# Kernel tuning notes

Measured on AMD Instinct MI355X. Metric: run time of the kernel, lower is better.

Reference implementation:

```python
import jax, jax.numpy as jnp
import numpy as np

EMBED_DIM = 1024
HEAD_SIZE = 64
N_HEAD = 16
N_QUERY_GROUPS = 4
SEQ_LEN = 2048
BATCH = 8


def setup_inputs() -> dict:
    key = jax.random.key(0)
    ks = jax.random.split(key, 7)
    s = 1.0 / np.sqrt(EMBED_DIM)
    x = jax.random.normal(ks[0], (BATCH, SEQ_LEN, EMBED_DIM), dtype=jnp.float32)
    Wq = jax.random.uniform(ks[1], (EMBED_DIM, N_HEAD * HEAD_SIZE), jnp.float32, -s, s)
    bq = jax.random.uniform(ks[2], (N_HEAD * HEAD_SIZE,), jnp.float32, -s, s)
    Wk = jax.random.uniform(ks[3], (EMBED_DIM, N_QUERY_GROUPS * HEAD_SIZE), jnp.float32, -s, s)
    bk = jax.random.uniform(ks[4], (N_QUERY_GROUPS * HEAD_SIZE,), jnp.float32, -s, s)
    Wv = jax.random.uniform(ks[5], (EMBED_DIM, N_QUERY_GROUPS * HEAD_SIZE), jnp.float32, -s, s)
    bv = jax.random.uniform(ks[6], (N_QUERY_GROUPS * HEAD_SIZE,), jnp.float32, -s, s)
    return {"x": x, "Wq": Wq, "bq": bq, "Wk": Wk, "bk": bk, "Wv": Wv, "bv": bv}


def reference(x, Wq, bq, Wk, bk, Wv, bv):
    B, T, _ = x.shape
    rep = N_HEAD // N_QUERY_GROUPS  # queries per group
    Q = x @ Wq + bq  # (B, T, H*hs)
    # GQA: torch .repeat tiles the group-block [g0..g3, g0..g3, ...]
    K = (x @ Wk + bk).reshape(B, T, N_QUERY_GROUPS, HEAD_SIZE)
    K = jnp.tile(K, (1, 1, rep, 1)).reshape(B, T, N_HEAD * HEAD_SIZE)
    V = (x @ Wv + bv).reshape(B, T, N_QUERY_GROUPS, HEAD_SIZE)
    V = jnp.tile(V, (1, 1, rep, 1)).reshape(B, T, N_HEAD * HEAD_SIZE)
    # flattened-head scores: contract over full H*hs dim (as in source)
    att = jnp.einsum('btd,bsd->bts', Q, K)  # (B, T, T)
    causal = jnp.triu(jnp.ones((T, T), dtype=bool), k=1)
    mask = jnp.where(causal, jnp.float32(-jnp.inf), jnp.float32(0.0))[None, None]  # (1,1,T,T)
    att = att + mask  # broadcasts to (1, B, T, T), matching torch semantics
    att = jax.nn.softmax(att, axis=-1) / jnp.sqrt(jnp.float32(HEAD_SIZE))  # post-hoc scale, as in source
    out = jnp.einsum('xbts,bsd->xbtd', att, V)  # (1, B, T, H*hs)
    return out
```

## Files before the change

kernel.cpp:

```cpp
#include <hip/hip_runtime.h>
#include <float.h>
#include <stdint.h>

#define T_ 2048
#define DG 256

typedef _Float16 half8 __attribute__((ext_vector_type(8)));
typedef _Float16 half4v __attribute__((ext_vector_type(4)));
typedef __fp16 fp16x2 __attribute__((ext_vector_type(2)));
typedef float f32x4 __attribute__((ext_vector_type(4)));
typedef float f32x16 __attribute__((ext_vector_type(16)));
typedef unsigned uint2v __attribute__((ext_vector_type(2)));

__device__ __forceinline__ void gload16(const void* g, void* l) {
  __builtin_amdgcn_global_load_lds(
      (const __attribute__((address_space(1))) unsigned int*)g,
      (__attribute__((address_space(3))) unsigned int*)l, 16, 0, 0);
}
#define WAIT_LGKM0() do { asm volatile("s_waitcnt lgkmcnt(0)" ::: "memory"); __builtin_amdgcn_sched_barrier(0); } while (0)

__device__ __forceinline__ float cross32(float x, int g) {
  unsigned u = __builtin_bit_cast(unsigned, x);
  uint2v r = __builtin_amdgcn_permlane32_swap(u, u, false, false);
  return __builtin_bit_cast(float, g ? r[0] : r[1]);
}

__global__ __launch_bounds__(256) void prep_w(
    const float* __restrict__ Wq, const float* __restrict__ bq,
    const float* __restrict__ Wk, const float* __restrict__ bk,
    const float* __restrict__ Wv, const float* __restrict__ bv,
    _Float16* __restrict__ Wt, float* __restrict__ bcat) {
  for (int idx = blockIdx.x * 256 + threadIdx.x; idx < 786432; idx += 768 * 256) {
    int n = idx >> 10, k = idx & 1023;
    float v;
    if (n < 256)      v = Wq[k * 1024 + n] + Wq[k * 1024 + n + 256]
                        + Wq[k * 1024 + n + 512] + Wq[k * 1024 + n + 768];
    else if (n < 512) v = Wk[k * 256 + n - 256];
    else              v = Wv[k * 256 + n - 512];
    Wt[idx] = (_Float16)v;
    if (k == 0) {
      float bb;
      if (n < 256)      bb = bq[n] + bq[n + 256] + bq[n + 512] + bq[n + 768];
      else if (n < 512) bb = bk[n - 256];
      else              bb = bv[n - 512];
      bcat[n] = bb;
    }
  }
}

__global__ __launch_bounds__(256) void xcvt(const float* __restrict__ x,
                                            _Float16* __restrict__ xh) {
  size_t i = (size_t)blockIdx.x * 256 + threadIdx.x;
  const float4* s = (const float4*)x + i * 2;
  float4 a = s[0], b = s[1];
  half8 h;
  h[0] = (_Float16)a.x; h[1] = (_Float16)a.y; h[2] = (_Float16)a.z; h[3] = (_Float16)a.w;
  h[4] = (_Float16)b.x; h[5] = (_Float16)b.y; h[6] = (_Float16)b.z; h[7] = (_Float16)b.w;
  *(half8*)(xh + i * 8) = h;
}

__global__ __launch_bounds__(256) void qkv_gemm(
    const _Float16* __restrict__ xh, const _Float16* __restrict__ Wt,
    const float* __restrict__ bcat,
    _Float16* __restrict__ Qh, _Float16* __restrict__ Kf, _Float16* __restrict__ Vf) {
  __shared__ __align__(16) uint8_t smem[32768];
  const int tid = threadIdx.x;
  const int w = tid >> 6, l = tid & 63;
  const int wr = w >> 1, wc = w & 1;
  const int lr = l & 15, lk = l >> 4;
  const int m0 = blockIdx.x * 128;
  const int by = blockIdx.y >> 1;
  const int nh = blockIdx.y & 1;

  f32x4 acc[4][4] = {};

  auto stage = [&](int k0, int buf) {
    uint8_t* Ab = smem + buf * 16384;
    uint8_t* Bb = Ab + 8192;
#pragma unroll
    for (int i = 0; i < 2; ++i) {
      int si = i * 256 + tid;
      int row = si >> 2, p = si & 3;
      gload16(xh + (size_t)(m0 + row) * 1024 + k0 + ((p ^ (row & 3)) << 3), Ab + si * 16);
    }
#pragma unroll
    for (int i = 0; i < 2; ++i) {
      int si = i * 256 + tid;
      int row = si >> 2, p = si & 3;
      gload16(Wt + (size_t)(by * 256 + nh * 128 + row) * 1024 + k0 + ((p ^ (row & 3)) << 3),
              Bb + si * 16);
    }
  };

  stage(0, 0);
  __syncthreads();

  for (int kt = 0; kt < 32; ++kt) {
    int cur = kt & 1;
    if (kt < 31) stage((kt + 1) * 32, cur ^ 1);
    const uint8_t* Ab = smem + cur * 16384;
    const uint8_t* Bb = Ab + 8192;
    half8 af[4], bf[4];
#pragma unroll
    for (int mi = 0; mi < 4; ++mi) {
      int row = wr * 64 + mi * 16 + lr;
      af[mi] = *(const half8*)(Ab + row * 64 + ((lk ^ (row & 3)) << 4));
    }
#pragma unroll
    for (int ni = 0; ni < 4; ++ni) {
      int row = wc * 64 + ni * 16 + lr;
      bf[ni] = *(const half8*)(Bb + row * 64 + ((lk ^ (row & 3)) << 4));
    }
#pragma unroll
    for (int mi = 0; mi < 4; ++mi)
#pragma unroll
      for (int ni = 0; ni < 4; ++ni)
        acc[mi][ni] = __builtin_amdgcn_mfma_f32_16x16x32_f16(af[mi], bf[ni], acc[mi][ni], 0, 0, 0);
    __syncthreads();
  }

  if (by == 0) {
#pragma unroll
    for (int mi = 0; mi < 4; ++mi)
#pragma unroll
      for (int ni = 0; ni < 4; ++ni) {
        int nl = nh * 128 + wc * 64 + ni * 16 + lr;
        int mg = m0 + wr * 64 + mi * 16 + lk * 4;
        float bias = bcat[nl];
#pragma unroll
        for (int r = 0; r < 4; ++r)
          Qh[(size_t)(mg + r) * DG + nl] = (_Float16)((acc[mi][ni][r] + bias) * 1.44269504f);
      }
  } else if (by == 2) {
#pragma unroll
    for (int mi = 0; mi < 4; ++mi)
#pragma unroll
      for (int ni = 0; ni < 4; ++ni) {
        int nl = nh * 128 + wc * 64 + ni * 16 + lr;
        int mg = m0 + wr * 64 + mi * 16 + lk * 4;
        float bias = bcat[512 + nl];
        int dt = nl >> 5, lnv = nl & 31;
        int bb = mg >> 11, t0 = mg & 2047;
        int st = t0 >> 5, sp = t0 & 31;
        int hs = sp >> 4, gg = (sp >> 3) & 1, j0 = sp & 7;
        size_t idx = (size_t)(((bb * 64 + st) * 8 + dt) * 2 + hs) * 512
                   + (gg * 32 + lnv) * 8 + j0;
        half4v h;
#pragma unroll
        for (int r = 0; r < 4; ++r) h[r] = (_Float16)(acc[mi][ni][r] + bias);
        *(half4v*)(Vf + idx) = h;
      }
  } else {
#pragma unroll
    for (int mi = 0; mi < 4; ++mi)
#pragma unroll
      for (int ni = 0; ni < 4; ++ni) {
        int dl = wc * 64 + ni * 16 + lr;
        float bias = bcat[256 + nh * 128 + dl];
#pragma unroll
        for (int r = 0; r < 4; ++r) {
          int t = wr * 64 + mi * 16 + lk * 4 + r;
          *(_Float16*)(smem + t * 256 + ((dl * 2) ^ ((t & 7) << 4))) =
              (_Float16)(acc[mi][ni][r] + bias);
        }
      }
    __syncthreads();
#pragma unroll
    for (int i = 0; i < 8; ++i) {
      int p = i * 256 + tid;
      int ln = p & 31, g = (p >> 5) & 1, cl = (p >> 6) & 7, st = p >> 9;
      int t = st * 32 + ln;
      int d0 = cl * 16 + g * 8;
      half8 v = *(const half8*)(smem + t * 256 + ((d0 * 2) ^ ((t & 7) << 4)));
      int tg = m0 + t;
      int bb = tg >> 11, stg = (tg & 2047) >> 5;
      int cc = nh * 8 + cl;
      *(half8*)(Kf + ((size_t)(((bb * 64 + stg) * 16 + cc) * 2 + g) * 32 + ln) * 8) = v;
    }
  }
}

__global__ __launch_bounds__(256, 4) void attn_main(
    const _Float16* __restrict__ Qg, const _Float16* __restrict__ Kf,
    const _Float16* __restrict__ Vf, float* __restrict__ out,
    _Float16* __restrict__ PO, float* __restrict__ ML) {
  __shared__ float Sx[5120];
  const int tid = threadIdx.x;
  const int wv = tid >> 6;
  const int l  = tid & 63;
  const int g  = l >> 5;
  const int ln = l & 31;
  const int id = blockIdx.x;
  const int b  = id & 7;
  const int u  = id >> 3;
  int tt, nc, c;
  if (u < 16)      { tt = u;                  nc = 1; c = 0; }
  else if (u < 48) { tt = 16 + ((u - 16) >> 1); nc = 2; c = (u - 16) & 1; }
  else if (u < 96) { tt = 32 + (u - 48) / 3;  nc = 3; c = (u - 48) % 3; }
  else             { tt = 48 + ((u - 96) >> 2); nc = 4; c = (u - 96) & 3; }
  const int len = (tt + nc) / nc;
  const int lo  = c * len;
  const int hi  = min(lo + len, tt + 1);
  const int q0  = tt * 32;

  const _Float16* Kfb = Kf + (size_t)b * 524288;
  const _Float16* Vfb = Vf + (size_t)b * 524288;

  const _Float16* Qrow = Qg + ((size_t)(b * T_ + q0 + ln)) * DG + wv * 64 + 8 * g;
  half8 qf[4];
#pragma unroll
  for (int j = 0; j < 4; ++j) qf[j] = *(const half8*)(Qrow + j * 16);

  f32x16 o0 = {}, o1 = {};
  float m_r = -1e30f, l_r = 0.0f;

  for (int kt = lo; kt < hi; ++kt) {
    const _Float16* kbase = Kfb + (size_t)(kt * 16 + 4 * wv) * 512 + l * 8;
    half8 kf0 = *(const half8*)(kbase);
    half8 kf1 = *(const half8*)(kbase + 512);
    half8 kf2 = *(const half8*)(kbase + 1024);
    half8 kf3 = *(const half8*)(kbase + 1536);
    const _Float16* vbase = Vfb + (size_t)(kt * 8 + 2 * wv) * 1024 + l * 8;
    half8 va0 = *(const half8*)(vbase);
    half8 va1 = *(const half8*)(vbase + 512);
    half8 vb0 = *(const half8*)(vbase + 1024);
    half8 vb1 = *(const half8*)(vbase + 1536);

    f32x16 s_acc = {};
    __builtin_amdgcn_s_setprio(1);
    s_acc = __builtin_amdgcn_mfma_f32_32x32x16_f16(kf0, qf[0], s_acc, 0, 0, 0);
    s_acc = __builtin_amdgcn_mfma_f32_32x32x16_f16(kf1, qf[1], s_acc, 0, 0, 0);
    s_acc = __builtin_amdgcn_mfma_f32_32x32x16_f16(kf2, qf[2], s_acc, 0, 0, 0);
    s_acc = __builtin_amdgcn_mfma_f32_32x32x16_f16(kf3, qf[3], s_acc, 0, 0, 0);
    __builtin_amdgcn_s_setprio(0);

    {
      float* myrow = Sx + (wv * 64 + l) * 20;
#pragma unroll
      for (int i = 0; i < 4; ++i)
        *(f32x4*)(myrow + 4 * i) = *(((const f32x4*)&s_acc) + i);
    }
    WAIT_LGKM0();
    __builtin_amdgcn_s_barrier();

    f32x4 sv[4];
#pragma unroll
    for (int i = 0; i < 4; ++i) sv[i] = *(((const f32x4*)&s_acc) + i);
#pragma unroll
    for (int wo = 0; wo < 4; ++wo) {
      if (wo == wv) continue;
      const float* prow = Sx + (wo * 64 + l) * 20;
#pragma unroll
      for (int i = 0; i < 4; ++i) sv[i] += *(const f32x4*)(prow + 4 * i);
    }
    float s[16];
#pragma unroll
    for (int r = 0; r < 16; ++r) s[r] = sv[r >> 2][r & 3];

    if (kt == tt) {
#pragma unroll
      for (int r = 0; r < 16; ++r) {
        int srow = (r & 3) + 8 * (r >> 2) + 4 * g;
        if (srow > ln) s[r] = -1e30f;
      }
    }
    float pmax = s[0];
#pragma unroll
    for (int r = 1; r < 16; ++r) pmax = fmaxf(pmax, s[r]);
    pmax = fmaxf(pmax, cross32(pmax, g));
    if (!__all(pmax <= m_r + 8.0f)) {
      float mnew = fmaxf(m_r, pmax);
      float sc = __builtin_amdgcn_exp2f(m_r - mnew);
      l_r *= sc;
#pragma unroll
      for (int r = 0; r < 16; ++r) { o0[r] *= sc; o1[r] *= sc; }
      m_r = mnew;
    }
    float p[16]; float psum = 0.0f;
#pragma unroll
    for (int r = 0; r < 16; ++r) { p[r] = __builtin_amdgcn_exp2f(s[r] - m_r); psum += p[r]; }
    l_r += psum + cross32(psum, g);

    unsigned ph[8];
#pragma unroll
    for (int i = 0; i < 8; ++i) {
      fp16x2 t2 = __builtin_amdgcn_cvt_pkrtz(p[2 * i], p[2 * i + 1]);
      ph[i] = __builtin_bit_cast(unsigned, t2);
    }
    union U { unsigned u[4]; half8 h; };
    U f0, f1;
    {
      uint2v r02 = __builtin_amdgcn_permlane32_swap(ph[0], ph[2], false, false);
      uint2v r13 = __builtin_amdgcn_permlane32_swap(ph[1], ph[3], false, false);
      uint2v r46 = __builtin_amdgcn_permlane32_swap(ph[4], ph[6], false, false);
      uint2v r57 = __builtin_amdgcn_permlane32_swap(ph[5], ph[7], false, false);
      f0.u[0] = r02[0]; f0.u[2] = r02[1];
      f0.u[1] = r13[0]; f0.u[3] = r13[1];
      f1.u[0] = r46[0]; f1.u[2] = r46[1];
      f1.u[1] = r57[0]; f1.u[3] = r57[1];
    }

    __builtin_amdgcn_s_setprio(1);
    o0 = __builtin_amdgcn_mfma_f32_32x32x16_f16(va0, f0.h, o0, 0, 0, 0);
    o0 = __builtin_amdgcn_mfma_f32_32x32x16_f16(va1, f1.h, o0, 0, 0, 0);
    o1 = __builtin_amdgcn_mfma_f32_32x32x16_f16(vb0, f0.h, o1, 0, 0, 0);
    o1 = __builtin_amdgcn_mfma_f32_32x32x16_f16(vb1, f1.h, o1, 0, 0, 0);
    __builtin_amdgcn_s_setprio(0);

    __builtin_amdgcn_s_barrier();
  }

  float* chunk = Sx + wv * 1280;
  if (nc == 1) {
    float inv = 1.0f / (l_r * 8.0f);
    float* ob = out + ((size_t)(b * T_ + q0)) * 1024;
#pragma unroll
    for (int dtl = 0; dtl < 2; ++dtl) {
      const f32x16& oo = dtl ? o1 : o0;
      WAIT_LGKM0();
#pragma unroll
      for (int r = 0; r < 16; ++r) {
        int dl = (r & 3) + 8 * (r >> 2) + 4 * g;
        chunk[ln * 33 + dl] = oo[r] * inv;
      }
      WAIT_LGKM0();
#pragma unroll
      for (int rr = 0; rr < 2; ++rr) {
        int qq = (l >> 2) + 16 * rr;
        int cp = (l & 3) * 8;
        float vv[8];
#pragma unroll
        for (int jj = 0; jj < 8; ++jj) vv[jj] = chunk[qq * 33 + cp + jj];
        float4 w0 = make_float4(vv[0], vv[1], vv[2], vv[3]);
        float4 w1 = make_float4(vv[4], vv[5], vv[6], vv[7]);
        float* orow = ob + (size_t)qq * 1024 + (2 * wv + dtl) * 32 + cp;
#pragma unroll
        for (int rep = 0; rep < 4; ++rep) {
          *(float4*)(orow + rep * 256)     = w0;
          *(float4*)(orow + rep * 256 + 4) = w1;
        }
      }
    }
  } else {
    int ti = tt - 16;
    int off = (ti < 16) ? ti * 2 : (ti < 32) ? 32 + (ti - 16) * 3 : 80 + (ti - 32) * 4;
    int slot = b * 144 + off + c;
    _Float16* P = PO + (size_t)slot * 8192;
#pragma unroll
    for (int dtl = 0; dtl < 2; ++dtl) {
      const f32x16& oo = dtl ? o1 : o0;
      WAIT_LGKM0();
#pragma unroll
      for (int r = 0; r < 16; ++r) {
        int dl = (r & 3) + 8 * (r >> 2) + 4 * g;
        chunk[ln * 33 + dl] = oo[r];
      }
      WAIT_LGKM0();
#pragma unroll
      for (int rr = 0; rr < 2; ++rr) {
        int qq = (l >> 2) + 16 * rr;
        int cp = (l & 3) * 8;
        half8 hv;
#pragma unroll
        for (int jj = 0; jj < 8; ++jj) hv[jj] = (_Float16)chunk[qq * 33 + cp + jj];
        *(half8*)(P + qq * 256 + (2 * wv + dtl) * 32 + cp) = hv;
      }
    }
    if (wv == 0 && l < 32) {
      ML[(size_t)slot * 64 + l]      = m_r;
      ML[(size_t)slot * 64 + 32 + l] = l_r;
    }
  }
}

__global__ __launch_bounds__(256) void attn_merge(
    const _Float16* __restrict__ PO, const float* __restrict__ ML,
    float* __restrict__ out) {
  const int id = blockIdx.x;
  const int b = id & 7, ti = id >> 3;
  const int tt = 16 + ti;
  const int nc = (ti < 16) ? 2 : (ti < 32) ? 3 : 4;
  const int off = (ti < 16) ? ti * 2 : (ti < 32) ? 32 + (ti - 16) * 3 : 80 + (ti - 32) * 4;
  const int slot0 = b * 144 + off;
  const int tid = threadIdx.x;
  const int row = tid >> 3, cb = tid & 7;

  float mj[4], lj[4];
  float M = -1e30f;
#pragma unroll
  for (int j = 0; j < 4; ++j)
    if (j < nc) {
      mj[j] = ML[(size_t)(slot0 + j) * 64 + row];
      lj[j] = ML[(size_t)(slot0 + j) * 64 + 32 + row];
      M = fmaxf(M, mj[j]);
    }
  float sc[4], lsum = 0.0f;
#pragma unroll
  for (int j = 0; j < 4; ++j)
    if (j < nc) { sc[j] = __builtin_amdgcn_exp2f(mj[j] - M); lsum += lj[j] * sc[j]; }
  float inv = 1.0f / (lsum * 8.0f);

  float acc[32] = {};
#pragma unroll
  for (int j = 0; j < 4; ++j)
    if (j < nc) {
      const _Float16* P = PO + (size_t)(slot0 + j) * 8192 + row * 256 + cb * 32;
      float s = sc[j];
#pragma unroll
      for (int q = 0; q < 4; ++q) {
        half8 h = *(const half8*)(P + q * 8);
#pragma unroll
        for (int e = 0; e < 8; ++e) acc[q * 8 + e] += s * (float)h[e];
      }
    }
  float* orow = out + ((size_t)(b * T_ + tt * 32 + row)) * 1024 + cb * 32;
#pragma unroll
  for (int q = 0; q < 8; ++q) {
    float4 v;
    v.x = acc[q * 4 + 0] * inv; v.y = acc[q * 4 + 1] * inv;
    v.z = acc[q * 4 + 2] * inv; v.w = acc[q * 4 + 3] * inv;
#pragma unroll
    for (int rep = 0; rep < 4; ++rep)
      *(float4*)(orow + rep * 256 + q * 4) = v;
  }
}

extern "C" void kernel_launch(void* const* d_in, const int* in_sizes, int n_in,
                              void* d_out, int out_size, void* d_ws, size_t ws_size,
                              hipStream_t stream) {
  const float* x  = (const float*)d_in[0];
  const float* Wq = (const float*)d_in[1];
  const float* bq = (const float*)d_in[2];
  const float* Wk = (const float*)d_in[3];
  const float* bk = (const float*)d_in[4];
  const float* Wv = (const float*)d_in[5];
  const float* bv = (const float*)d_in[6];
  float* out = (float*)d_out;
  char* ws = (char*)d_ws;
  _Float16* Wt   = (_Float16*)ws;
  float*    bcat = (float*)(ws + 0x180000);
  _Float16* Qh   = (_Float16*)(ws + 0x181000);
  _Float16* Kf   = (_Float16*)(ws + 0x981000);
  _Float16* Vf   = (_Float16*)(ws + 0x1181000);
  _Float16* xh   = (_Float16*)(ws + 0x1981000);
  _Float16* PO   = (_Float16*)(ws + 0x1981000);
  float*    ML   = (float*)(ws + 0x1981000 + 0x1200000);

  prep_w<<<768, 256, 0, stream>>>(Wq, bq, Wk, bk, Wv, bv, Wt, bcat);
  xcvt<<<8192, 256, 0, stream>>>(x, xh);
  qkv_gemm<<<dim3(128, 6), 256, 0, stream>>>(xh, Wt, bcat, Qh, Kf, Vf);
  attn_main<<<1280, 256, 0, stream>>>(Qh, Kf, Vf, out, PO, ML);
  attn_merge<<<384, 256, 0, stream>>>(PO, ML, out);
}
```

Before: 156.8 us.

## Fuse fp32-to-fp16 conversion of x into QKV GEMM and widen N tile

Removes the separate xcvt kernel and its fp16 copy of x: the GEMM now reads fp32 x through registers, converts with packed round-toward-zero conversions, and writes the fp16 tile to LDS one iteration ahead. The N tile doubles to 256 so each block covers a whole Q/K/V section, which halves the grid and means x is read from global memory once per section instead of twice. This trades a full extra pass over x for more accumulator registers, a larger LDS footprint, fewer blocks, and a two-phase K epilogue. The conversion also changes rounding from round-to-nearest to round-toward-zero.

```diff
diff --git a/kernel.cpp b/kernel.cpp
--- a/kernel.cpp
+++ b/kernel.cpp
@@ -23,6 +23,15 @@
   unsigned u = __builtin_bit_cast(unsigned, x);
   uint2v r = __builtin_amdgcn_permlane32_swap(u, u, false, false);
   return __builtin_bit_cast(float, g ? r[0] : r[1]);
+}
+
+__device__ __forceinline__ half8 cvt8(float4 a, float4 b) {
+  union { unsigned u[4]; half8 h; } r;
+  r.u[0] = __builtin_bit_cast(unsigned, __builtin_amdgcn_cvt_pkrtz(a.x, a.y));
+  r.u[1] = __builtin_bit_cast(unsigned, __builtin_amdgcn_cvt_pkrtz(a.z, a.w));
+  r.u[2] = __builtin_bit_cast(unsigned, __builtin_amdgcn_cvt_pkrtz(b.x, b.y));
+  r.u[3] = __builtin_bit_cast(unsigned, __builtin_amdgcn_cvt_pkrtz(b.z, b.w));
+  return r.h;
 }
 
 __global__ __launch_bounds__(256) void prep_w(
@@ -48,74 +57,74 @@
   }
 }
 
-__global__ __launch_bounds__(256) void xcvt(const float* __restrict__ x,
-                                            _Float16* __restrict__ xh) {
-  size_t i = (size_t)blockIdx.x * 256 + threadIdx.x;
-  const float4* s = (const float4*)x + i * 2;
-  float4 a = s[0], b = s[1];
-  half8 h;
-  h[0] = (_Float16)a.x; h[1] = (_Float16)a.y; h[2] = (_Float16)a.z; h[3] = (_Float16)a.w;
-  h[4] = (_Float16)b.x; h[5] = (_Float16)b.y; h[6] = (_Float16)b.z; h[7] = (_Float16)b.w;
-  *(half8*)(xh + i * 8) = h;
-}
-
 __global__ __launch_bounds__(256) void qkv_gemm(
-    const _Float16* __restrict__ xh, const _Float16* __restrict__ Wt,
+    const float* __restrict__ x, const _Float16* __restrict__ Wt,
     const float* __restrict__ bcat,
     _Float16* __restrict__ Qh, _Float16* __restrict__ Kf, _Float16* __restrict__ Vf) {
-  __shared__ __align__(16) uint8_t smem[32768];
+  __shared__ __align__(16) uint8_t smem[49152];
   const int tid = threadIdx.x;
   const int w = tid >> 6, l = tid & 63;
   const int wr = w >> 1, wc = w & 1;
   const int lr = l & 15, lk = l >> 4;
   const int m0 = blockIdx.x * 128;
-  const int by = blockIdx.y >> 1;
-  const int nh = blockIdx.y & 1;
-
-  f32x4 acc[4][4] = {};
-
-  auto stage = [&](int k0, int buf) {
-    uint8_t* Ab = smem + buf * 16384;
-    uint8_t* Bb = Ab + 8192;
-#pragma unroll
-    for (int i = 0; i < 2; ++i) {
+  const int by = blockIdx.y;
+  const int n0 = by * 256;
+
+  f32x4 acc[4][8] = {};
+
+  const int arow = tid >> 1;
+  const int ag   = (tid & 1) * 2;
+
+  auto loadA = [&](int k0, float4* fr) {
+    const float4* src = (const float4*)(x + (size_t)(m0 + arow) * 1024 + k0 + ag * 8);
+    fr[0] = src[0]; fr[1] = src[1]; fr[2] = src[2]; fr[3] = src[3];
+  };
+  auto writeA = [&](int buf, const float4* fr) {
+    uint8_t* Ab = smem + buf * 24576;
+    *(half8*)(Ab + arow * 64 + (((ag + 0) ^ (arow & 3)) << 4)) = cvt8(fr[0], fr[1]);
+    *(half8*)(Ab + arow * 64 + (((ag + 1) ^ (arow & 3)) << 4)) = cvt8(fr[2], fr[3]);
+  };
+  auto stageB = [&](int k0, int buf) {
+    uint8_t* Bb = smem + buf * 24576 + 8192;
+#pragma unroll
+    for (int i = 0; i < 4; ++i) {
       int si = i * 256 + tid;
       int row = si >> 2, p = si & 3;
-      gload16(xh + (size_t)(m0 + row) * 1024 + k0 + ((p ^ (row & 3)) << 3), Ab + si * 16);
-    }
-#pragma unroll
-    for (int i = 0; i < 2; ++i) {
-      int si = i * 256 + tid;
-      int row = si >> 2, p = si & 3;
-      gload16(Wt + (size_t)(by * 256 + nh * 128 + row) * 1024 + k0 + ((p ^ (row & 3)) << 3),
-              Bb + si * 16);
+      gload16(Wt + (size_t)(n0 + row) * 1024 + k0 + ((p ^ (row & 3)) << 3), Bb + si * 16);
     }
   };
 
-  stage(0, 0);
+  {
+    float4 fr[4];
+    loadA(0, fr);
+    stageB(0, 0);
+    writeA(0, fr);
+  }
   __syncthreads();
 
   for (int kt = 0; kt < 32; ++kt) {
     int cur = kt & 1;
-    if (kt < 31) stage((kt + 1) * 32, cur ^ 1);
-    const uint8_t* Ab = smem + cur * 16384;
+    float4 nf[4];
+    if (kt < 31) { loadA((kt + 1) * 32, nf); stageB((kt + 1) * 32, cur ^ 1); }
+    const uint8_t* Ab = smem + cur * 24576;
     const uint8_t* Bb = Ab + 8192;
-    half8 af[4], bf[4];
+    half8 af[4], bf[8];
 #pragma unroll
     for (int mi = 0; mi < 4; ++mi) {
       int row = wr * 64 + mi * 16 + lr;
       af[mi] = *(const half8*)(Ab + row * 64 + ((lk ^ (row & 3)) << 4));
     }
 #pragma unroll
-    for (int ni = 0; ni < 4; ++ni) {
-      int row = wc * 64 + ni * 16 + lr;
+    for (int ni = 0; ni < 8; ++ni) {
+      int row = wc * 128 + ni * 16 + lr;
       bf[ni] = *(const half8*)(Bb + row * 64 + ((lk ^ (row & 3)) << 4));
     }
 #pragma unroll
     for (int mi = 0; mi < 4; ++mi)
 #pragma unroll
-      for (int ni = 0; ni < 4; ++ni)
+      for (int ni = 0; ni < 8; ++ni)
         acc[mi][ni] = __builtin_amdgcn_mfma_f32_16x16x32_f16(af[mi], bf[ni], acc[mi][ni], 0, 0, 0);
+    if (kt < 31) writeA(cur ^ 1, nf);
     __syncthreads();
   }
 
@@ -123,8 +132,8 @@
 #pragma unroll
     for (int mi = 0; mi < 4; ++mi)
 #pragma unroll
-      for (int ni = 0; ni < 4; ++ni) {
-        int nl = nh * 128 + wc * 64 + ni * 16 + lr;
+      for (int ni = 0; ni < 8; ++ni) {
+        int nl = wc * 128 + ni * 16 + lr;
         int mg = m0 + wr * 64 + mi * 16 + lk * 4;
         float bias = bcat[nl];
 #pragma unroll
@@ -135,8 +144,8 @@
 #pragma unroll
     for (int mi = 0; mi < 4; ++mi)
 #pragma unroll
-      for (int ni = 0; ni < 4; ++ni) {
-        int nl = nh * 128 + wc * 64 + ni * 16 + lr;
+      for (int ni = 0; ni < 8; ++ni) {
+        int nl = wc * 128 + ni * 16 + lr;
         int mg = m0 + wr * 64 + mi * 16 + lk * 4;
         float bias = bcat[512 + nl];
         int dt = nl >> 5, lnv = nl & 31;
@@ -152,30 +161,36 @@
       }
   } else {
 #pragma unroll
-    for (int mi = 0; mi < 4; ++mi)
-#pragma unroll
-      for (int ni = 0; ni < 4; ++ni) {
-        int dl = wc * 64 + ni * 16 + lr;
-        float bias = bcat[256 + nh * 128 + dl];
-#pragma unroll
-        for (int r = 0; r < 4; ++r) {
-          int t = wr * 64 + mi * 16 + lk * 4 + r;
-          *(_Float16*)(smem + t * 256 + ((dl * 2) ^ ((t & 7) << 4))) =
-              (_Float16)(acc[mi][ni][r] + bias);
-        }
-      }
-    __syncthreads();
-#pragma unroll
-    for (int i = 0; i < 8; ++i) {
-      int p = i * 256 + tid;
-      int ln = p & 31, g = (p >> 5) & 1, cl = (p >> 6) & 7, st = p >> 9;
-      int t = st * 32 + ln;
-      int d0 = cl * 16 + g * 8;
-      half8 v = *(const half8*)(smem + t * 256 + ((d0 * 2) ^ ((t & 7) << 4)));
-      int tg = m0 + t;
-      int bb = tg >> 11, stg = (tg & 2047) >> 5;
-      int cc = nh * 8 + cl;
-      *(half8*)(Kf + ((size_t)(((bb * 64 + stg) * 16 + cc) * 2 + g) * 32 + ln) * 8) = v;
+    for (int h = 0; h < 2; ++h) {
+      if (wc == h) {
+#pragma unroll
+        for (int mi = 0; mi < 4; ++mi)
+#pragma unroll
+          for (int ni = 0; ni < 8; ++ni) {
+            int dl = ni * 16 + lr;
+            float bias = bcat[256 + h * 128 + dl];
+#pragma unroll
+            for (int r = 0; r < 4; ++r) {
+              int t = wr * 64 + mi * 16 + lk * 4 + r;
+              *(_Float16*)(smem + t * 256 + ((dl * 2) ^ ((t & 7) << 4))) =
+                  (_Float16)(acc[mi][ni][r] + bias);
+            }
+          }
+      }
+      __syncthreads();
+#pragma unroll
+      for (int i = 0; i < 8; ++i) {
+        int p = i * 256 + tid;
+        int ln = p & 31, g = (p >> 5) & 1, cl = (p >> 6) & 7, st = p >> 9;
+        int t = st * 32 + ln;
+        int d0 = cl * 16 + g * 8;
+        half8 v = *(const half8*)(smem + t * 256 + ((d0 * 2) ^ ((t & 7) << 4)));
+        int tg = m0 + t;
+        int bb = tg >> 11, stg = (tg & 2047) >> 5;
+        int cc = h * 8 + cl;
+        *(half8*)(Kf + ((size_t)(((bb * 64 + stg) * 16 + cc) * 2 + g) * 32 + ln) * 8) = v;
+      }
+      __syncthreads();
     }
   }
 }
@@ -442,13 +457,11 @@
   _Float16* Qh   = (_Float16*)(ws + 0x181000);
   _Float16* Kf   = (_Float16*)(ws + 0x981000);
   _Float16* Vf   = (_Float16*)(ws + 0x1181000);
-  _Float16* xh   = (_Float16*)(ws + 0x1981000);
   _Float16* PO   = (_Float16*)(ws + 0x1981000);
   float*    ML   = (float*)(ws + 0x1981000 + 0x1200000);
 
   prep_w<<<768, 256, 0, stream>>>(Wq, bq, Wk, bk, Wv, bv, Wt, bcat);
-  xcvt<<<8192, 256, 0, stream>>>(x, xh);
-  qkv_gemm<<<dim3(128, 6), 256, 0, stream>>>(xh, Wt, bcat, Qh, Kf, Vf);
+  qkv_gemm<<<dim3(128, 3), 256, 0, stream>>>(x, Wt, bcat, Qh, Kf, Vf);
   attn_main<<<1280, 256, 0, stream>>>(Qh, Kf, Vf, out, PO, ML);
   attn_merge<<<384, 256, 0, stream>>>(PO, ML, out);
 }
```

Result: slower. 185.6 us (+18.3%).

## Fuse weight prep into x conversion; centralize softmax in wave 0 with LDS broadcast

Applied to the files above, without the earlier changes.

Merges the weight-transpose/fold kernel into the x fp16 conversion kernel, removing one launch. In attention, only wave 0 reduces the split-K score partials and computes the softmax. It then publishes the fp16 probabilities, rescale factors and a rescale flag through shared memory, and the other waves read them after an extra barrier. This removes redundant softmax work across four waves, but adds a second block barrier per key tile and serializes the softmax on one wave.

```diff
diff --git a/kernel.cpp b/kernel.cpp
--- a/kernel.cpp
+++ b/kernel.cpp
@@ -25,19 +25,27 @@
   return __builtin_bit_cast(float, g ? r[0] : r[1]);
 }
 
-__global__ __launch_bounds__(256) void prep_w(
+__global__ __launch_bounds__(256) void prepx(
+    const float* __restrict__ x,
     const float* __restrict__ Wq, const float* __restrict__ bq,
     const float* __restrict__ Wk, const float* __restrict__ bk,
     const float* __restrict__ Wv, const float* __restrict__ bv,
-    _Float16* __restrict__ Wt, float* __restrict__ bcat) {
-  for (int idx = blockIdx.x * 256 + threadIdx.x; idx < 786432; idx += 768 * 256) {
-    int n = idx >> 10, k = idx & 1023;
+    _Float16* __restrict__ xh, _Float16* __restrict__ Wt, float* __restrict__ bcat) {
+  size_t t = (size_t)blockIdx.x * 256 + threadIdx.x;
+  const float4* s = (const float4*)x + t * 2;
+  float4 a = s[0], b = s[1];
+  half8 h;
+  h[0] = (_Float16)a.x; h[1] = (_Float16)a.y; h[2] = (_Float16)a.z; h[3] = (_Float16)a.w;
+  h[4] = (_Float16)b.x; h[5] = (_Float16)b.y; h[6] = (_Float16)b.z; h[7] = (_Float16)b.w;
+  *(half8*)(xh + t * 8) = h;
+  if (t < 786432) {
+    int n = (int)(t >> 10), k = (int)(t & 1023);
     float v;
     if (n < 256)      v = Wq[k * 1024 + n] + Wq[k * 1024 + n + 256]
                         + Wq[k * 1024 + n + 512] + Wq[k * 1024 + n + 768];
     else if (n < 512) v = Wk[k * 256 + n - 256];
     else              v = Wv[k * 256 + n - 512];
-    Wt[idx] = (_Float16)v;
+    Wt[t] = (_Float16)v;
     if (k == 0) {
       float bb;
       if (n < 256)      bb = bq[n] + bq[n + 256] + bq[n + 512] + bq[n + 768];
@@ -46,17 +54,6 @@
       bcat[n] = bb;
     }
   }
-}
-
-__global__ __launch_bounds__(256) void xcvt(const float* __restrict__ x,
-                                            _Float16* __restrict__ xh) {
-  size_t i = (size_t)blockIdx.x * 256 + threadIdx.x;
-  const float4* s = (const float4*)x + i * 2;
-  float4 a = s[0], b = s[1];
-  half8 h;
-  h[0] = (_Float16)a.x; h[1] = (_Float16)a.y; h[2] = (_Float16)a.z; h[3] = (_Float16)a.w;
-  h[4] = (_Float16)b.x; h[5] = (_Float16)b.y; h[6] = (_Float16)b.z; h[7] = (_Float16)b.w;
-  *(half8*)(xh + i * 8) = h;
 }
 
 __global__ __launch_bounds__(256) void qkv_gemm(
@@ -185,6 +182,10 @@
     const _Float16* __restrict__ Vf, float* __restrict__ out,
     _Float16* __restrict__ PO, float* __restrict__ ML) {
   __shared__ float Sx[5120];
+  __shared__ __align__(16) _Float16 Pl[1024];
+  __shared__ float SC[64];
+  __shared__ float INV[64];
+  __shared__ int Flg;
   const int tid = threadIdx.x;
   const int wv = tid >> 6;
   const int l  = tid & 63;
@@ -234,7 +235,7 @@
     s_acc = __builtin_amdgcn_mfma_f32_32x32x16_f16(kf3, qf[3], s_acc, 0, 0, 0);
     __builtin_amdgcn_s_setprio(0);
 
-    {
+    if (wv != 0) {
       float* myrow = Sx + (wv * 64 + l) * 20;
 #pragma unroll
       for (int i = 0; i < 4; ++i)
@@ -243,76 +244,109 @@
     WAIT_LGKM0();
     __builtin_amdgcn_s_barrier();
 
-    f32x4 sv[4];
-#pragma unroll
-    for (int i = 0; i < 4; ++i) sv[i] = *(((const f32x4*)&s_acc) + i);
-#pragma unroll
-    for (int wo = 0; wo < 4; ++wo) {
-      if (wo == wv) continue;
-      const float* prow = Sx + (wo * 64 + l) * 20;
-#pragma unroll
-      for (int i = 0; i < 4; ++i) sv[i] += *(const f32x4*)(prow + 4 * i);
-    }
-    float s[16];
-#pragma unroll
-    for (int r = 0; r < 16; ++r) s[r] = sv[r >> 2][r & 3];
-
-    if (kt == tt) {
-#pragma unroll
-      for (int r = 0; r < 16; ++r) {
-        int srow = (r & 3) + 8 * (r >> 2) + 4 * g;
-        if (srow > ln) s[r] = -1e30f;
-      }
-    }
-    float pmax = s[0];
-#pragma unroll
-    for (int r = 1; r < 16; ++r) pmax = fmaxf(pmax, s[r]);
-    pmax = fmaxf(pmax, cross32(pmax, g));
-    if (!__all(pmax <= m_r + 8.0f)) {
-      float mnew = fmaxf(m_r, pmax);
-      float sc = __builtin_amdgcn_exp2f(m_r - mnew);
-      l_r *= sc;
-#pragma unroll
-      for (int r = 0; r < 16; ++r) { o0[r] *= sc; o1[r] *= sc; }
-      m_r = mnew;
-    }
-    float p[16]; float psum = 0.0f;
-#pragma unroll
-    for (int r = 0; r < 16; ++r) { p[r] = __builtin_amdgcn_exp2f(s[r] - m_r); psum += p[r]; }
-    l_r += psum + cross32(psum, g);
-
-    unsigned ph[8];
-#pragma unroll
-    for (int i = 0; i < 8; ++i) {
-      fp16x2 t2 = __builtin_amdgcn_cvt_pkrtz(p[2 * i], p[2 * i + 1]);
-      ph[i] = __builtin_bit_cast(unsigned, t2);
-    }
-    union U { unsigned u[4]; half8 h; };
-    U f0, f1;
-    {
-      uint2v r02 = __builtin_amdgcn_permlane32_swap(ph[0], ph[2], false, false);
-      uint2v r13 = __builtin_amdgcn_permlane32_swap(ph[1], ph[3], false, false);
-      uint2v r46 = __builtin_amdgcn_permlane32_swap(ph[4], ph[6], false, false);
-      uint2v r57 = __builtin_amdgcn_permlane32_swap(ph[5], ph[7], false, false);
-      f0.u[0] = r02[0]; f0.u[2] = r02[1];
-      f0.u[1] = r13[0]; f0.u[3] = r13[1];
-      f1.u[0] = r46[0]; f1.u[2] = r46[1];
-      f1.u[1] = r57[0]; f1.u[3] = r57[1];
+    half8 f0h, f1h;
+    if (wv == 0) {
+      f32x4 sv[4];
+#pragma unroll
+      for (int i = 0; i < 4; ++i) sv[i] = *(((const f32x4*)&s_acc) + i);
+#pragma unroll
+      for (int wo = 1; wo < 4; ++wo) {
+        const float* prow = Sx + (wo * 64 + l) * 20;
+#pragma unroll
+        for (int i = 0; i < 4; ++i) sv[i] += *(const f32x4*)(prow + 4 * i);
+      }
+      float s[16];
+#pragma unroll
+      for (int r = 0; r < 16; ++r) s[r] = sv[r >> 2][r & 3];
+      if (kt == tt) {
+#pragma unroll
+        for (int r = 0; r < 16; ++r) {
+          int srow = (r & 3) + 8 * (r >> 2) + 4 * g;
+          if (srow > ln) s[r] = -1e30f;
+        }
+      }
+      float pmax = s[0];
+#pragma unroll
+      for (int r = 1; r < 16; ++r) pmax = fmaxf(pmax, s[r]);
+      pmax = fmaxf(pmax, cross32(pmax, g));
+      int doresc = !__all(pmax <= m_r + 8.0f);
+      float scl = 1.0f;
+      if (doresc) {
+        float mnew = fmaxf(m_r, pmax);
+        scl = __builtin_amdgcn_exp2f(m_r - mnew);
+        l_r *= scl;
+#pragma unroll
+        for (int r = 0; r < 16; ++r) { o0[r] *= scl; o1[r] *= scl; }
+        m_r = mnew;
+      }
+      if (l == 0) Flg = doresc;
+      SC[l] = scl;
+      float p[16]; float psum = 0.0f;
+#pragma unroll
+      for (int r = 0; r < 16; ++r) { p[r] = __builtin_amdgcn_exp2f(s[r] - m_r); psum += p[r]; }
+      l_r += psum + cross32(psum, g);
+      unsigned ph[8];
+#pragma unroll
+      for (int i = 0; i < 8; ++i) {
+        fp16x2 t2 = __builtin_amdgcn_cvt_pkrtz(p[2 * i], p[2 * i + 1]);
+        ph[i] = __builtin_bit_cast(unsigned, t2);
+      }
+      union U { unsigned u[4]; half8 h; };
+      U w0, w1;
+      w0.u[0] = ph[0]; w0.u[1] = ph[1]; w0.u[2] = ph[2]; w0.u[3] = ph[3];
+      w1.u[0] = ph[4]; w1.u[1] = ph[5]; w1.u[2] = ph[6]; w1.u[3] = ph[7];
+      *(half8*)&Pl[l * 16]     = w0.h;
+      *(half8*)&Pl[l * 16 + 8] = w1.h;
+      U f0, f1;
+      {
+        uint2v r02 = __builtin_amdgcn_permlane32_swap(ph[0], ph[2], false, false);
+        uint2v r13 = __builtin_amdgcn_permlane32_swap(ph[1], ph[3], false, false);
+        uint2v r46 = __builtin_amdgcn_permlane32_swap(ph[4], ph[6], false, false);
+        uint2v r57 = __builtin_amdgcn_permlane32_swap(ph[5], ph[7], false, false);
+        f0.u[0] = r02[0]; f0.u[2] = r02[1];
+        f0.u[1] = r13[0]; f0.u[3] = r13[1];
+        f1.u[0] = r46[0]; f1.u[2] = r46[1];
+        f1.u[1] = r57[0]; f1.u[3] = r57[1];
+      }
+      f0h = f0.h; f1h = f1.h;
+    }
+    WAIT_LGKM0();
+    __builtin_amdgcn_s_barrier();
+
+    if (wv != 0) {
+      int dr = Flg;
+      if (dr) {
+        float scl = SC[l];
+#pragma unroll
+        for (int r = 0; r < 16; ++r) { o0[r] *= scl; o1[r] *= scl; }
+      }
+      union V8 { half4v v[2]; half8 h; } F0, F1;
+      const _Float16* base0 = &Pl[ln * 16];
+      const _Float16* base1 = &Pl[(32 + ln) * 16];
+      F0.v[0] = *(const half4v*)(base0 + 4 * g);
+      F0.v[1] = *(const half4v*)(base1 + 4 * g);
+      F1.v[0] = *(const half4v*)(base0 + 8 + 4 * g);
+      F1.v[1] = *(const half4v*)(base1 + 8 + 4 * g);
+      f0h = F0.h; f1h = F1.h;
     }
 
     __builtin_amdgcn_s_setprio(1);
-    o0 = __builtin_amdgcn_mfma_f32_32x32x16_f16(va0, f0.h, o0, 0, 0, 0);
-    o0 = __builtin_amdgcn_mfma_f32_32x32x16_f16(va1, f1.h, o0, 0, 0, 0);
-    o1 = __builtin_amdgcn_mfma_f32_32x32x16_f16(vb0, f0.h, o1, 0, 0, 0);
-    o1 = __builtin_amdgcn_mfma_f32_32x32x16_f16(vb1, f1.h, o1, 0, 0, 0);
+    o0 = __builtin_amdgcn_mfma_f32_32x32x16_f16(va0, f0h, o0, 0, 0, 0);
+    o0 = __builtin_amdgcn_mfma_f32_32x32x16_f16(va1, f1h, o0, 0, 0, 0);
+    o1 = __builtin_amdgcn_mfma_f32_32x32x16_f16(vb0, f0h, o1, 0, 0, 0);
+    o1 = __builtin_amdgcn_mfma_f32_32x32x16_f16(vb1, f1h, o1, 0, 0, 0);
     __builtin_amdgcn_s_setprio(0);
 
     __builtin_amdgcn_s_barrier();
   }
+
+  if (wv == 0) INV[l] = 1.0f / (l_r * 8.0f);
+  WAIT_LGKM0();
+  __builtin_amdgcn_s_barrier();
+  float inv = INV[l];
 
   float* chunk = Sx + wv * 1280;
   if (nc == 1) {
-    float inv = 1.0f / (l_r * 8.0f);
     float* ob = out + ((size_t)(b * T_ + q0)) * 1024;
 #pragma unroll
     for (int dtl = 0; dtl < 2; ++dtl) {
@@ -446,8 +480,7 @@
   _Float16* PO   = (_Float16*)(ws + 0x1981000);
   float*    ML   = (float*)(ws + 0x1981000 + 0x1200000);
 
-  prep_w<<<768, 256, 0, stream>>>(Wq, bq, Wk, bk, Wv, bv, Wt, bcat);
-  xcvt<<<8192, 256, 0, stream>>>(x, xh);
+  prepx<<<8192, 256, 0, stream>>>(x, Wq, bq, Wk, bk, Wv, bv, xh, Wt, bcat);
   qkv_gemm<<<dim3(128, 6), 256, 0, stream>>>(xh, Wt, bcat, Qh, Kf, Vf);
   attn_main<<<1280, 256, 0, stream>>>(Qh, Kf, Vf, out, PO, ML);
   attn_merge<<<384, 256, 0, stream>>>(PO, ML, out);
```

After: 151.0 us. -3.7%, faster.
